# Kernel optimization log

Hardware: AMD Instinct MI355X
Metric: run time of the kernel (lower is better)

## Reference

```python
import jax, jax.numpy as jnp
import numpy as np

N = 50000        # nodes
E = 800000       # edges (before self loops)
F_IN = 64        # num_features
DIM = 64         # num_hidden
C = 10           # num_classes
G = 256          # graphs in batch
NEG_SLOPE = 0.2


def setup_inputs() -> dict:
    key = jax.random.key(0)
    ks = jax.random.split(key, 20)
    def w(k, shape, fan_in):
        return jax.random.normal(k, shape, dtype=jnp.float32) / np.sqrt(fan_in)
    x = jax.random.normal(ks[0], (N, F_IN), dtype=jnp.float32)
    edge_index = jax.random.randint(ks[1], (2, E), 0, N, dtype=jnp.int64)
    batch = jnp.sort(jax.random.randint(ks[2], (N,), 0, G, dtype=jnp.int64))
    return {
        "x": x, "edge_index": edge_index, "batch": batch,
        "w1": w(ks[3], (F_IN, DIM), F_IN), "as1": w(ks[4], (DIM,), DIM), "ad1": w(ks[5], (DIM,), DIM), "b1": jnp.zeros((DIM,), jnp.float32),
        "w2": w(ks[6], (DIM, DIM), DIM),  "as2": w(ks[7], (DIM,), DIM), "ad2": w(ks[8], (DIM,), DIM), "b2": jnp.zeros((DIM,), jnp.float32),
        "w3": w(ks[9], (DIM, DIM), DIM),  "as3": w(ks[10], (DIM,), DIM), "ad3": w(ks[11], (DIM,), DIM), "b3": jnp.zeros((DIM,), jnp.float32),
        "fc1_w": w(ks[12], (DIM, DIM), DIM), "fc1_b": jnp.zeros((DIM,), jnp.float32),
        "fc2_w": w(ks[13], (DIM, C), DIM),   "fc2_b": jnp.zeros((C,), jnp.float32),
    }


def _gat_conv(x, src, dst, w, a_src, a_dst, b, n_nodes):
    # PyG GATConv, heads=1: h = x W; e_ij = LeakyReLU(a_src.h_j + a_dst.h_i);
    # alpha = segment-softmax over edges grouped by target i; out_i = sum_j alpha_ij h_j + b
    h = x @ w                                   # [N, DIM]
    alpha_s = h @ a_src                         # [N]
    alpha_d = h @ a_dst                         # [N]
    e = jax.nn.leaky_relu(alpha_s[src] + alpha_d[dst], NEG_SLOPE)  # [E']
    e_max = jax.ops.segment_max(e, dst, num_segments=n_nodes)
    e_exp = jnp.exp(e - e_max[dst])
    denom = jax.ops.segment_sum(e_exp, dst, num_segments=n_nodes)
    alpha = e_exp / (denom[dst] + 1e-16)        # [E']
    out = jax.ops.segment_sum(alpha[:, None] * h[src], dst, num_segments=n_nodes)
    return out + b


def _l2_normalize(x):
    nrm = jnp.linalg.norm(x, axis=1, keepdims=True)
    return x / jnp.maximum(nrm, 1e-12)


def reference(x, edge_index, batch, w1, as1, ad1, b1, w2, as2, ad2, b2,
              w3, as3, ad3, b3, fc1_w, fc1_b, fc2_w, fc2_b):
    n = x.shape[0]
    loops = jnp.arange(n, dtype=edge_index.dtype)
    src = jnp.concatenate([edge_index[0], loops])   # add_self_loops=True (PyG default)
    dst = jnp.concatenate([edge_index[1], loops])
    h = _gat_conv(x, src, dst, w1, as1, ad1, b1, n)
    h = jax.nn.relu(_l2_normalize(h))
    h = _gat_conv(h, src, dst, w2, as2, ad2, b2, n)
    h = jax.nn.relu(_l2_normalize(h))
    h = _gat_conv(h, src, dst, w3, as3, ad3, b3, n)
    h = jax.nn.relu(_l2_normalize(h))
    g = jax.ops.segment_sum(h, batch, num_segments=G)   # global_add_pool -> [G, DIM]
    g = jax.nn.relu(g @ fc1_w + fc1_b)
    logits = g @ fc2_w + fc2_b
    return jax.nn.log_softmax(logits, axis=-1)
```

## Files before the change

kernel.cpp:

```cpp
#include <hip/hip_runtime.h>
#include <hip/hip_bf16.h>
#include <math.h>

#define DIM 64
#define GNUM 256
#define CNUM 10

__device__ __forceinline__ unsigned bfpack(float a, float b) {
    unsigned ua = __builtin_bit_cast(unsigned, a);
    unsigned ub = __builtin_bit_cast(unsigned, b);
    ua += 0x7fffu + ((ua >> 16) & 1u);
    ub += 0x7fffu + ((ub >> 16) & 1u);
    return (ua >> 16) | (ub & 0xffff0000u);
}
__device__ __forceinline__ float bflo(unsigned u) { return __builtin_bit_cast(float, u << 16); }
__device__ __forceinline__ float bfhi(unsigned u) { return __builtin_bit_cast(float, u & 0xffff0000u); }

__global__ void deg_rank_kernel(const int* __restrict__ ei, int E, int N,
                                int* __restrict__ deg, int* __restrict__ rank) {
    int i = blockIdx.x * blockDim.x + threadIdx.x;
    int EP = E + N;
    if (i >= EP) return;
    int d = (i < E) ? ei[E + i] : (i - E);
    rank[i] = atomicAdd(&deg[d], 1);
}

__global__ __launch_bounds__(256) void scan_misc(const int* __restrict__ deg, int* __restrict__ part, int n, int nb,
                                                 const int* __restrict__ batch, int N,
                                                 int* __restrict__ gstart) {
    int bid = blockIdx.x;
    if (bid < nb) {
        __shared__ int ws[4];
        int i = bid * 256 + threadIdx.x;
        int v = (i < n) ? deg[i] : 0;
        #pragma unroll
        for (int d = 32; d >= 1; d >>= 1) v += __shfl_xor(v, d);
        if ((threadIdx.x & 63) == 0) ws[threadIdx.x >> 6] = v;
        __syncthreads();
        if (threadIdx.x == 0) part[bid] = ws[0] + ws[1] + ws[2] + ws[3];
    } else {
        for (int g = threadIdx.x; g <= GNUM; g += 256) {
            int lo = 0, hi = N;
            while (lo < hi) { int mid = (lo + hi) >> 1; if (batch[mid] < g) lo = mid + 1; else hi = mid; }
            gstart[g] = lo;
        }
    }
}

__global__ __launch_bounds__(256) void scan_down(const int* __restrict__ deg, const int* __restrict__ part,
                                                 int* __restrict__ offs, int n) {
    __shared__ int ws[4];
    __shared__ int base_s;
    int tid = threadIdx.x, lane = tid & 63, wid = tid >> 6;
    int pv = (tid < (int)blockIdx.x) ? part[tid] : 0;
    #pragma unroll
    for (int d = 32; d >= 1; d >>= 1) pv += __shfl_xor(pv, d);
    if (lane == 0) ws[wid] = pv;
    __syncthreads();
    if (tid == 0) base_s = ws[0] + ws[1] + ws[2] + ws[3];
    __syncthreads();
    int i = blockIdx.x * 256 + tid;
    int v = (i < n) ? deg[i] : 0;
    int x = v;
    #pragma unroll
    for (int d = 1; d < 64; d <<= 1) { int t = __shfl_up(x, d); if (lane >= d) x += t; }
    if (lane == 63) ws[wid] = x;
    __syncthreads();
    int add = base_s;
    for (int w = 0; w < wid; ++w) add += ws[w];
    if (i < n) offs[i] = add + x - v;
    if (i == n - 1) offs[n] = add + x;
}

#define XSTR 68
__device__ __forceinline__ void mm_tile_body(int bid,
                                             const float* __restrict__ in, const float* __restrict__ W,
                                             const float* __restrict__ a_s, const float* __restrict__ a_d,
                                             unsigned* __restrict__ hb, float* __restrict__ as_,
                                             float* __restrict__ ad_, int N) {
    __shared__ float Ws[DIM * DIM];
    __shared__ float xT[XSTR * DIM];
    int tid = threadIdx.x;
    int base = bid * 64;

    const float4* W4 = (const float4*)W;
    float4* Ws4 = (float4*)Ws;
    #pragma unroll
    for (int i = 0; i < 4; ++i) Ws4[tid + 256 * i] = W4[tid + 256 * i];

    {
        int row = tid >> 2;
        int kb = (tid & 3) << 4;
        int grow = base + row;
        int crow = grow < N ? grow : N - 1;
        const float4* xr = (const float4*)(in + ((size_t)crow << 6) + kb);
        float4 v0 = xr[0], v1 = xr[1], v2 = xr[2], v3 = xr[3];
        xT[(kb + 0) * XSTR + row] = v0.x;  xT[(kb + 1) * XSTR + row] = v0.y;
        xT[(kb + 2) * XSTR + row] = v0.z;  xT[(kb + 3) * XSTR + row] = v0.w;
        xT[(kb + 4) * XSTR + row] = v1.x;  xT[(kb + 5) * XSTR + row] = v1.y;
        xT[(kb + 6) * XSTR + row] = v1.z;  xT[(kb + 7) * XSTR + row] = v1.w;
        xT[(kb + 8) * XSTR + row] = v2.x;  xT[(kb + 9) * XSTR + row] = v2.y;
        xT[(kb + 10) * XSTR + row] = v2.z; xT[(kb + 11) * XSTR + row] = v2.w;
        xT[(kb + 12) * XSTR + row] = v3.x; xT[(kb + 13) * XSTR + row] = v3.y;
        xT[(kb + 14) * XSTR + row] = v3.z; xT[(kb + 15) * XSTR + row] = v3.w;
    }
    __syncthreads();

    int tx = tid & 15, ty = tid >> 4;
    int c0 = tx << 2, r0 = ty << 2;
    float acc[4][4] = {{0.f}};
    #pragma unroll 8
    for (int k = 0; k < DIM; ++k) {
        float4 xv = *(const float4*)(xT + k * XSTR + r0);
        float4 wv = *(const float4*)(Ws + k * DIM + c0);
        acc[0][0] += xv.x * wv.x; acc[0][1] += xv.x * wv.y; acc[0][2] += xv.x * wv.z; acc[0][3] += xv.x * wv.w;
        acc[1][0] += xv.y * wv.x; acc[1][1] += xv.y * wv.y; acc[1][2] += xv.y * wv.z; acc[1][3] += xv.y * wv.w;
        acc[2][0] += xv.z * wv.x; acc[2][1] += xv.z * wv.y; acc[2][2] += xv.z * wv.z; acc[2][3] += xv.z * wv.w;
        acc[3][0] += xv.w * wv.x; acc[3][1] += xv.w * wv.y; acc[3][2] += xv.w * wv.z; acc[3][3] += xv.w * wv.w;
    }

    float4 av = *(const float4*)(a_s + c0);
    float4 dv = *(const float4*)(a_d + c0);
    #pragma unroll
    for (int ri = 0; ri < 4; ++ri) {
        int grow = base + r0 + ri;
        float s1 = acc[ri][0] * av.x + acc[ri][1] * av.y + acc[ri][2] * av.z + acc[ri][3] * av.w;
        float s2 = acc[ri][0] * dv.x + acc[ri][1] * dv.y + acc[ri][2] * dv.z + acc[ri][3] * dv.w;
        #pragma unroll
        for (int d = 1; d <= 8; d <<= 1) { s1 += __shfl_xor(s1, d); s2 += __shfl_xor(s2, d); }
        if (grow < N) {
            uint2 o;
            o.x = bfpack(acc[ri][0], acc[ri][1]);
            o.y = bfpack(acc[ri][2], acc[ri][3]);
            *(uint2*)(hb + ((size_t)grow << 5) + (tx << 1)) = o;
            if (tx == 0) { as_[grow] = s1; ad_[grow] = s2; }
        }
    }
}

__global__ __launch_bounds__(256) void mm_tile(const float* __restrict__ in, const float* __restrict__ W,
                                               const float* __restrict__ a_s, const float* __restrict__ a_d,
                                               unsigned* __restrict__ hb, float* __restrict__ as_,
                                               float* __restrict__ ad_, int N) {
    mm_tile_body(blockIdx.x, in, W, a_s, a_d, hb, as_, ad_, N);
}

__global__ __launch_bounds__(256) void mm_fill(const float* __restrict__ in, const float* __restrict__ W,
                                               const float* __restrict__ a_s, const float* __restrict__ a_d,
                                               unsigned* __restrict__ hb, float* __restrict__ as_,
                                               float* __restrict__ ad_, int N, int nbt,
                                               const int* __restrict__ ei, const int* __restrict__ rank, int E,
                                               const int* __restrict__ offs, int* __restrict__ csr_src) {
    int bid = blockIdx.x;
    if (bid < nbt) {
        mm_tile_body(bid, in, W, a_s, a_d, hb, as_, ad_, N);
    } else {
        int i = (bid - nbt) * 256 + threadIdx.x;
        int EP = E + N;
        if (i >= EP) return;
        int s, d;
        if (i < E) { s = ei[i]; d = ei[E + i]; } else { s = i - E; d = i - E; }
        csr_src[offs[d] + rank[i]] = s;
    }
}

__global__ __launch_bounds__(256) void gat_agg(const unsigned* __restrict__ hb, const float* __restrict__ as_,
                                               const float* __restrict__ ad_, const int* __restrict__ offs,
                                               const int* __restrict__ csr, const float* __restrict__ bias,
                                               float* __restrict__ out, int N) {
    int tid = threadIdx.x, lane = tid & 63, wid = tid >> 6;
    int node = blockIdx.x * 4 + wid;
    if (node >= N) return;
    int start = offs[node], end = offs[node + 1];
    int deg = end - start;
    float adi = ad_[node];

    int src_reg = 0;
    float e_reg = -1e30f;
    if (lane < deg) {
        src_reg = csr[start + lane];
        float e = as_[src_reg] + adi;
        e_reg = (e > 0.f) ? e : 0.2f * e;
    }
    float m = e_reg;
    for (int t = start + 64 + lane; t < end; t += 64) {
        float e = as_[csr[t]] + adi;
        e = (e > 0.f) ? e : 0.2f * e;
        m = fmaxf(m, e);
    }
    #pragma unroll
    for (int d = 32; d >= 1; d >>= 1) m = fmaxf(m, __shfl_xor(m, d));

    float w_reg = (lane < deg) ? expf(e_reg - m) : 0.f;
    float s = w_reg;
    for (int t = start + 64 + lane; t < end; t += 64) {
        float e = as_[csr[t]] + adi;
        e = (e > 0.f) ? e : 0.2f * e;
        s += expf(e - m);
    }
    #pragma unroll
    for (int d = 32; d >= 1; d >>= 1) s += __shfl_xor(s, d);

    int esub = lane >> 4, fg = lane & 15;
    int dmain = deg < 64 ? deg : 64;
    float a0 = 0.f, a1 = 0.f, a2 = 0.f, a3 = 0.f;
    for (int i0 = 0; i0 < dmain; i0 += 16) {
        float wA = __shfl(w_reg, i0 + esub);
        int   sA = __shfl(src_reg, i0 + esub);
        float wB = __shfl(w_reg, i0 + 4 + esub);
        int   sB = __shfl(src_reg, i0 + 4 + esub);
        float wC = __shfl(w_reg, i0 + 8 + esub);
        int   sC = __shfl(src_reg, i0 + 8 + esub);
        float wD = __shfl(w_reg, i0 + 12 + esub);
        int   sD = __shfl(src_reg, i0 + 12 + esub);
        const uint2 hA = *(const uint2*)(hb + ((size_t)sA << 5) + (fg << 1));
        const uint2 hB = *(const uint2*)(hb + ((size_t)sB << 5) + (fg << 1));
        const uint2 hC = *(const uint2*)(hb + ((size_t)sC << 5) + (fg << 1));
        const uint2 hD = *(const uint2*)(hb + ((size_t)sD << 5) + (fg << 1));
        a0 += wA * bflo(hA.x) + wB * bflo(hB.x) + wC * bflo(hC.x) + wD * bflo(hD.x);
        a1 += wA * bfhi(hA.x) + wB * bfhi(hB.x) + wC * bfhi(hC.x) + wD * bfhi(hD.x);
        a2 += wA * bflo(hA.y) + wB * bflo(hB.y) + wC * bflo(hC.y) + wD * bflo(hD.y);
        a3 += wA * bfhi(hA.y) + wB * bfhi(hB.y) + wC * bfhi(hC.y) + wD * bfhi(hD.y);
    }
    for (int t0 = start + 64; t0 < end; t0 += 4) {
        int t = t0 + esub;
        float w = 0.f; int src = 0;
        if (t < end) {
            src = csr[t];
            float e = as_[src] + adi;
            e = (e > 0.f) ? e : 0.2f * e;
            w = expf(e - m);
        }
        const uint2 hv = *(const uint2*)(hb + ((size_t)src << 5) + (fg << 1));
        a0 += w * bflo(hv.x); a1 += w * bfhi(hv.x);
        a2 += w * bflo(hv.y); a3 += w * bfhi(hv.y);
    }
    #pragma unroll
    for (int d = 16; d <= 32; d <<= 1) {
        a0 += __shfl_xor(a0, d); a1 += __shfl_xor(a1, d);
        a2 += __shfl_xor(a2, d); a3 += __shfl_xor(a3, d);
    }
    float inv = 1.f / (s + 1e-16f);
    const float4 bv = *(const float4*)(bias + (fg << 2));
    float o0 = a0 * inv + bv.x, o1 = a1 * inv + bv.y, o2 = a2 * inv + bv.z, o3 = a3 * inv + bv.w;
    float n2 = o0 * o0 + o1 * o1 + o2 * o2 + o3 * o3;
    #pragma unroll
    for (int d = 1; d <= 8; d <<= 1) n2 += __shfl_xor(n2, d);
    float innrm = 1.f / fmaxf(sqrtf(n2), 1e-12f);
    if (esub == 0) {
        float4 o;
        o.x = fmaxf(o0 * innrm, 0.f); o.y = fmaxf(o1 * innrm, 0.f);
        o.z = fmaxf(o2 * innrm, 0.f); o.w = fmaxf(o3 * innrm, 0.f);
        *(float4*)(out + ((size_t)node << 6) + (fg << 2)) = o;
    }
}

__global__ __launch_bounds__(256) void pool_mlp(const float* __restrict__ h, const int* __restrict__ gstart,
                                                const float* __restrict__ fc1w, const float* __restrict__ fc1b,
                                                const float* __restrict__ fc2w, const float* __restrict__ fc2b,
                                                float* __restrict__ out) {
    __shared__ float W1[DIM * DIM];
    __shared__ float red[4 * DIM];
    __shared__ float tbuf[DIM];
    __shared__ float obuf[CNUM];
    int tid = threadIdx.x, lane = tid & 63, wv = tid >> 6;
    int gid = blockIdx.x;

    const float4* W4 = (const float4*)fc1w;
    float4* W1s = (float4*)W1;
    #pragma unroll
    for (int i = 0; i < 4; ++i) W1s[tid + 256 * i] = W4[tid + 256 * i];

    int s = gstart[gid], e = gstart[gid + 1];
    float acc = 0.f;
    for (int i = s + wv; i < e; i += 4) acc += h[((size_t)i << 6) + lane];
    red[wv * DIM + lane] = acc;
    __syncthreads();

    if (wv == 0) {
        float g = red[lane] + red[DIM + lane] + red[2 * DIM + lane] + red[3 * DIM + lane];
        float t = fc1b[lane];
        #pragma unroll
        for (int k = 0; k < DIM; ++k) t += __shfl(g, k) * W1[k * DIM + lane];
        t = fmaxf(t, 0.f);
        tbuf[lane] = t;
        float o = 0.f;
        if (lane < CNUM) {
            o = fc2b[lane];
            #pragma unroll
            for (int k = 0; k < DIM; ++k) o += tbuf[k] * fc2w[k * CNUM + lane];
            obuf[lane] = o;
        }
        if (lane < CNUM) {
            float mx = obuf[0];
            #pragma unroll
            for (int k = 1; k < CNUM; ++k) mx = fmaxf(mx, obuf[k]);
            float ssum = 0.f;
            #pragma unroll
            for (int k = 0; k < CNUM; ++k) ssum += expf(obuf[k] - mx);
            out[gid * CNUM + lane] = o - mx - logf(ssum);
        }
    }
}

static inline size_t align256(size_t x) { return (x + 255) & ~size_t(255); }

extern "C" void kernel_launch(void* const* d_in, const int* in_sizes, int n_in,
                              void* d_out, int out_size, void* d_ws, size_t ws_size,
                              hipStream_t stream) {
    const float* x     = (const float*)d_in[0];
    const int*   ei    = (const int*)d_in[1];
    const int*   batch = (const int*)d_in[2];
    const float* w1  = (const float*)d_in[3];
    const float* as1 = (const float*)d_in[4];
    const float* ad1 = (const float*)d_in[5];
    const float* b1  = (const float*)d_in[6];
    const float* w2  = (const float*)d_in[7];
    const float* as2 = (const float*)d_in[8];
    const float* ad2 = (const float*)d_in[9];
    const float* b2  = (const float*)d_in[10];
    const float* w3  = (const float*)d_in[11];
    const float* as3 = (const float*)d_in[12];
    const float* ad3 = (const float*)d_in[13];
    const float* b3  = (const float*)d_in[14];
    const float* fc1w = (const float*)d_in[15];
    const float* fc1b = (const float*)d_in[16];
    const float* fc2w = (const float*)d_in[17];
    const float* fc2b = (const float*)d_in[18];
    float* out = (float*)d_out;

    int N  = in_sizes[0] / DIM;
    int E  = in_sizes[1] / 2;
    int EP = E + N;
    int nb = (N + 255) / 256;

    char* p = (char*)d_ws;
    unsigned* hbf = (unsigned*)p; p += align256(sizeof(unsigned) * (size_t)N * (DIM / 2));
    float* oA   = (float*)p; p += align256(sizeof(float) * (size_t)N * DIM);
    float* oB   = (float*)p; p += align256(sizeof(float) * (size_t)N * DIM);
    float* as_  = (float*)p; p += align256(sizeof(float) * (size_t)N);
    float* ad_  = (float*)p; p += align256(sizeof(float) * (size_t)N);
    int*   deg  = (int*)p;   p += align256(sizeof(int) * (size_t)N);
    int*   offs = (int*)p;   p += align256(sizeof(int) * (size_t)(N + 1));
    int*   rank = (int*)p;   p += align256(sizeof(int) * (size_t)EP);
    int*   csr  = (int*)p;   p += align256(sizeof(int) * (size_t)EP);
    int*   part = (int*)p;   p += align256(sizeof(int) * (size_t)nb);
    int*   gst  = (int*)p;   p += align256(sizeof(int) * (size_t)(GNUM + 1));

    int nblk = (N + 3) / 4;
    int nbt = (N + 63) / 64;
    int epBlocks = (EP + 255) / 256;

    hipMemsetAsync(deg, 0, sizeof(int) * (size_t)N, stream);
    deg_rank_kernel<<<epBlocks, 256, 0, stream>>>(ei, E, N, deg, rank);
    scan_misc<<<nb + 1, 256, 0, stream>>>(deg, part, N, nb, batch, N, gst);
    scan_down<<<nb, 256, 0, stream>>>(deg, part, offs, N);

    mm_fill<<<nbt + epBlocks, 256, 0, stream>>>(x, w1, as1, ad1, hbf, as_, ad_, N, nbt,
                                                ei, rank, E, offs, csr);
    gat_agg<<<nblk, 256, 0, stream>>>(hbf, as_, ad_, offs, csr, b1, oA, N);
    mm_tile<<<nbt, 256, 0, stream>>>(oA, w2, as2, ad2, hbf, as_, ad_, N);
    gat_agg<<<nblk, 256, 0, stream>>>(hbf, as_, ad_, offs, csr, b2, oB, N);
    mm_tile<<<nbt, 256, 0, stream>>>(oB, w3, as3, ad3, hbf, as_, ad_, N);
    gat_agg<<<nblk, 256, 0, stream>>>(hbf, as_, ad_, offs, csr, b3, oA, N);

    pool_mlp<<<GNUM, 256, 0, stream>>>(oA, gst, fc1w, fc1b, fc2w, fc2b, out);
}
```

Before: 290.2 us.

## Store inter-layer activations as bf16 and drop softmax max pass

The GAT aggregation now writes its normalized, ReLU'd output as packed bf16 instead of fp32. The following matmul tiles and the pooling kernel read bf16 directly, which halves the intermediate activation traffic. The segment softmax no longer computes a per-node max or a separate denominator pass. It exponentiates raw logits and accumulates the sum inside the gather loop, removing the shuffle reductions and the extra loops over high-degree nodes. The cost is lower precision in intermediates and a possible exp overflow if attention logits get large.

```diff
diff --git a/kernel.cpp b/kernel.cpp
--- a/kernel.cpp
+++ b/kernel.cpp
@@ -15,6 +15,7 @@
 }
 __device__ __forceinline__ float bflo(unsigned u) { return __builtin_bit_cast(float, u << 16); }
 __device__ __forceinline__ float bfhi(unsigned u) { return __builtin_bit_cast(float, u & 0xffff0000u); }
+__device__ __forceinline__ float bfs(unsigned short u) { return __builtin_bit_cast(float, (unsigned)u << 16); }
 
 __global__ void deg_rank_kernel(const int* __restrict__ ei, int E, int N,
                                 int* __restrict__ deg, int* __restrict__ rank) {
@@ -73,8 +74,9 @@
 }
 
 #define XSTR 68
+template<bool BF16IN>
 __device__ __forceinline__ void mm_tile_body(int bid,
-                                             const float* __restrict__ in, const float* __restrict__ W,
+                                             const void* __restrict__ in_, const float* __restrict__ W,
                                              const float* __restrict__ a_s, const float* __restrict__ a_d,
                                              unsigned* __restrict__ hb, float* __restrict__ as_,
                                              float* __restrict__ ad_, int N) {
@@ -93,16 +95,30 @@
         int kb = (tid & 3) << 4;
         int grow = base + row;
         int crow = grow < N ? grow : N - 1;
-        const float4* xr = (const float4*)(in + ((size_t)crow << 6) + kb);
-        float4 v0 = xr[0], v1 = xr[1], v2 = xr[2], v3 = xr[3];
-        xT[(kb + 0) * XSTR + row] = v0.x;  xT[(kb + 1) * XSTR + row] = v0.y;
-        xT[(kb + 2) * XSTR + row] = v0.z;  xT[(kb + 3) * XSTR + row] = v0.w;
-        xT[(kb + 4) * XSTR + row] = v1.x;  xT[(kb + 5) * XSTR + row] = v1.y;
-        xT[(kb + 6) * XSTR + row] = v1.z;  xT[(kb + 7) * XSTR + row] = v1.w;
-        xT[(kb + 8) * XSTR + row] = v2.x;  xT[(kb + 9) * XSTR + row] = v2.y;
-        xT[(kb + 10) * XSTR + row] = v2.z; xT[(kb + 11) * XSTR + row] = v2.w;
-        xT[(kb + 12) * XSTR + row] = v3.x; xT[(kb + 13) * XSTR + row] = v3.y;
-        xT[(kb + 14) * XSTR + row] = v3.z; xT[(kb + 15) * XSTR + row] = v3.w;
+        if (BF16IN) {
+            const unsigned* xr = (const unsigned*)in_ + ((size_t)crow << 5) + (kb >> 1);
+            uint4 u0 = *(const uint4*)xr;
+            uint4 u1 = *(const uint4*)(xr + 4);
+            xT[(kb + 0) * XSTR + row] = bflo(u0.x);  xT[(kb + 1) * XSTR + row] = bfhi(u0.x);
+            xT[(kb + 2) * XSTR + row] = bflo(u0.y);  xT[(kb + 3) * XSTR + row] = bfhi(u0.y);
+            xT[(kb + 4) * XSTR + row] = bflo(u0.z);  xT[(kb + 5) * XSTR + row] = bfhi(u0.z);
+            xT[(kb + 6) * XSTR + row] = bflo(u0.w);  xT[(kb + 7) * XSTR + row] = bfhi(u0.w);
+            xT[(kb + 8) * XSTR + row] = bflo(u1.x);  xT[(kb + 9) * XSTR + row] = bfhi(u1.x);
+            xT[(kb + 10) * XSTR + row] = bflo(u1.y); xT[(kb + 11) * XSTR + row] = bfhi(u1.y);
+            xT[(kb + 12) * XSTR + row] = bflo(u1.z); xT[(kb + 13) * XSTR + row] = bfhi(u1.z);
+            xT[(kb + 14) * XSTR + row] = bflo(u1.w); xT[(kb + 15) * XSTR + row] = bfhi(u1.w);
+        } else {
+            const float4* xr = (const float4*)((const float*)in_ + ((size_t)crow << 6) + kb);
+            float4 v0 = xr[0], v1 = xr[1], v2 = xr[2], v3 = xr[3];
+            xT[(kb + 0) * XSTR + row] = v0.x;  xT[(kb + 1) * XSTR + row] = v0.y;
+            xT[(kb + 2) * XSTR + row] = v0.z;  xT[(kb + 3) * XSTR + row] = v0.w;
+            xT[(kb + 4) * XSTR + row] = v1.x;  xT[(kb + 5) * XSTR + row] = v1.y;
+            xT[(kb + 6) * XSTR + row] = v1.z;  xT[(kb + 7) * XSTR + row] = v1.w;
+            xT[(kb + 8) * XSTR + row] = v2.x;  xT[(kb + 9) * XSTR + row] = v2.y;
+            xT[(kb + 10) * XSTR + row] = v2.z; xT[(kb + 11) * XSTR + row] = v2.w;
+            xT[(kb + 12) * XSTR + row] = v3.x; xT[(kb + 13) * XSTR + row] = v3.y;
+            xT[(kb + 14) * XSTR + row] = v3.z; xT[(kb + 15) * XSTR + row] = v3.w;
+        }
     }
     __syncthreads();
 
@@ -138,11 +154,11 @@
     }
 }
 
-__global__ __launch_bounds__(256) void mm_tile(const float* __restrict__ in, const float* __restrict__ W,
-                                               const float* __restrict__ a_s, const float* __restrict__ a_d,
-                                               unsigned* __restrict__ hb, float* __restrict__ as_,
-                                               float* __restrict__ ad_, int N) {
-    mm_tile_body(blockIdx.x, in, W, a_s, a_d, hb, as_, ad_, N);
+__global__ __launch_bounds__(256) void mm_tile_bf(const unsigned* __restrict__ in, const float* __restrict__ W,
+                                                  const float* __restrict__ a_s, const float* __restrict__ a_d,
+                                                  unsigned* __restrict__ hb, float* __restrict__ as_,
+                                                  float* __restrict__ ad_, int N) {
+    mm_tile_body<true>(blockIdx.x, in, W, a_s, a_d, hb, as_, ad_, N);
 }
 
 __global__ __launch_bounds__(256) void mm_fill(const float* __restrict__ in, const float* __restrict__ W,
@@ -153,7 +169,7 @@
                                                const int* __restrict__ offs, int* __restrict__ csr_src) {
     int bid = blockIdx.x;
     if (bid < nbt) {
-        mm_tile_body(bid, in, W, a_s, a_d, hb, as_, ad_, N);
+        mm_tile_body<false>(bid, in, W, a_s, a_d, hb, as_, ad_, N);
     } else {
         int i = (bid - nbt) * 256 + threadIdx.x;
         int EP = E + N;
@@ -167,7 +183,7 @@
 __global__ __launch_bounds__(256) void gat_agg(const unsigned* __restrict__ hb, const float* __restrict__ as_,
                                                const float* __restrict__ ad_, const int* __restrict__ offs,
                                                const int* __restrict__ csr, const float* __restrict__ bias,
-                                               float* __restrict__ out, int N) {
+                                               unsigned* __restrict__ outb, int N) {
     int tid = threadIdx.x, lane = tid & 63, wid = tid >> 6;
     int node = blockIdx.x * 4 + wid;
     if (node >= N) return;
@@ -176,34 +192,17 @@
     float adi = ad_[node];
 
     int src_reg = 0;
-    float e_reg = -1e30f;
+    float w_reg = 0.f;
     if (lane < deg) {
         src_reg = csr[start + lane];
         float e = as_[src_reg] + adi;
-        e_reg = (e > 0.f) ? e : 0.2f * e;
-    }
-    float m = e_reg;
-    for (int t = start + 64 + lane; t < end; t += 64) {
-        float e = as_[csr[t]] + adi;
         e = (e > 0.f) ? e : 0.2f * e;
-        m = fmaxf(m, e);
-    }
-    #pragma unroll
-    for (int d = 32; d >= 1; d >>= 1) m = fmaxf(m, __shfl_xor(m, d));
-
-    float w_reg = (lane < deg) ? expf(e_reg - m) : 0.f;
-    float s = w_reg;
-    for (int t = start + 64 + lane; t < end; t += 64) {
-        float e = as_[csr[t]] + adi;
-        e = (e > 0.f) ? e : 0.2f * e;
-        s += expf(e - m);
-    }
-    #pragma unroll
-    for (int d = 32; d >= 1; d >>= 1) s += __shfl_xor(s, d);
+        w_reg = expf(e);
+    }
 
     int esub = lane >> 4, fg = lane & 15;
     int dmain = deg < 64 ? deg : 64;
-    float a0 = 0.f, a1 = 0.f, a2 = 0.f, a3 = 0.f;
+    float a0 = 0.f, a1 = 0.f, a2 = 0.f, a3 = 0.f, sw = 0.f;
     for (int i0 = 0; i0 < dmain; i0 += 16) {
         float wA = __shfl(w_reg, i0 + esub);
         int   sA = __shfl(src_reg, i0 + esub);
@@ -217,6 +216,7 @@
         const uint2 hB = *(const uint2*)(hb + ((size_t)sB << 5) + (fg << 1));
         const uint2 hC = *(const uint2*)(hb + ((size_t)sC << 5) + (fg << 1));
         const uint2 hD = *(const uint2*)(hb + ((size_t)sD << 5) + (fg << 1));
+        sw += wA + wB + wC + wD;
         a0 += wA * bflo(hA.x) + wB * bflo(hB.x) + wC * bflo(hC.x) + wD * bflo(hD.x);
         a1 += wA * bfhi(hA.x) + wB * bfhi(hB.x) + wC * bfhi(hC.x) + wD * bfhi(hD.x);
         a2 += wA * bflo(hA.y) + wB * bflo(hB.y) + wC * bflo(hC.y) + wD * bflo(hD.y);
@@ -229,9 +229,10 @@
             src = csr[t];
             float e = as_[src] + adi;
             e = (e > 0.f) ? e : 0.2f * e;
-            w = expf(e - m);
+            w = expf(e);
         }
         const uint2 hv = *(const uint2*)(hb + ((size_t)src << 5) + (fg << 1));
+        sw += w;
         a0 += w * bflo(hv.x); a1 += w * bfhi(hv.x);
         a2 += w * bflo(hv.y); a3 += w * bfhi(hv.y);
     }
@@ -239,8 +240,9 @@
     for (int d = 16; d <= 32; d <<= 1) {
         a0 += __shfl_xor(a0, d); a1 += __shfl_xor(a1, d);
         a2 += __shfl_xor(a2, d); a3 += __shfl_xor(a3, d);
-    }
-    float inv = 1.f / (s + 1e-16f);
+        sw += __shfl_xor(sw, d);
+    }
+    float inv = 1.f / (sw + 1e-16f);
     const float4 bv = *(const float4*)(bias + (fg << 2));
     float o0 = a0 * inv + bv.x, o1 = a1 * inv + bv.y, o2 = a2 * inv + bv.z, o3 = a3 * inv + bv.w;
     float n2 = o0 * o0 + o1 * o1 + o2 * o2 + o3 * o3;
@@ -248,14 +250,14 @@
     for (int d = 1; d <= 8; d <<= 1) n2 += __shfl_xor(n2, d);
     float innrm = 1.f / fmaxf(sqrtf(n2), 1e-12f);
     if (esub == 0) {
-        float4 o;
-        o.x = fmaxf(o0 * innrm, 0.f); o.y = fmaxf(o1 * innrm, 0.f);
-        o.z = fmaxf(o2 * innrm, 0.f); o.w = fmaxf(o3 * innrm, 0.f);
-        *(float4*)(out + ((size_t)node << 6) + (fg << 2)) = o;
-    }
-}
-
-__global__ __launch_bounds__(256) void pool_mlp(const float* __restrict__ h, const int* __restrict__ gstart,
+        uint2 o;
+        o.x = bfpack(fmaxf(o0 * innrm, 0.f), fmaxf(o1 * innrm, 0.f));
+        o.y = bfpack(fmaxf(o2 * innrm, 0.f), fmaxf(o3 * innrm, 0.f));
+        *(uint2*)(outb + ((size_t)node << 5) + (fg << 1)) = o;
+    }
+}
+
+__global__ __launch_bounds__(256) void pool_mlp(const unsigned short* __restrict__ hb, const int* __restrict__ gstart,
                                                 const float* __restrict__ fc1w, const float* __restrict__ fc1b,
                                                 const float* __restrict__ fc2w, const float* __restrict__ fc2b,
                                                 float* __restrict__ out) {
@@ -273,7 +275,7 @@
 
     int s = gstart[gid], e = gstart[gid + 1];
     float acc = 0.f;
-    for (int i = s + wv; i < e; i += 4) acc += h[((size_t)i << 6) + lane];
+    for (int i = s + wv; i < e; i += 4) acc += bfs(hb[((size_t)i << 6) + lane]);
     red[wv * DIM + lane] = acc;
     __syncthreads();
 
@@ -336,8 +338,8 @@
 
     char* p = (char*)d_ws;
     unsigned* hbf = (unsigned*)p; p += align256(sizeof(unsigned) * (size_t)N * (DIM / 2));
-    float* oA   = (float*)p; p += align256(sizeof(float) * (size_t)N * DIM);
-    float* oB   = (float*)p; p += align256(sizeof(float) * (size_t)N * DIM);
+    unsigned* oAb = (unsigned*)p; p += align256(sizeof(unsigned) * (size_t)N * (DIM / 2));
+    unsigned* oBb = (unsigned*)p; p += align256(sizeof(unsigned) * (size_t)N * (DIM / 2));
     float* as_  = (float*)p; p += align256(sizeof(float) * (size_t)N);
     float* ad_  = (float*)p; p += align256(sizeof(float) * (size_t)N);
     int*   deg  = (int*)p;   p += align256(sizeof(int) * (size_t)N);
@@ -358,11 +360,11 @@
 
     mm_fill<<<nbt + epBlocks, 256, 0, stream>>>(x, w1, as1, ad1, hbf, as_, ad_, N, nbt,
                                                 ei, rank, E, offs, csr);
-    gat_agg<<<nblk, 256, 0, stream>>>(hbf, as_, ad_, offs, csr, b1, oA, N);
-    mm_tile<<<nbt, 256, 0, stream>>>(oA, w2, as2, ad2, hbf, as_, ad_, N);
-    gat_agg<<<nblk, 256, 0, stream>>>(hbf, as_, ad_, offs, csr, b2, oB, N);
-    mm_tile<<<nbt, 256, 0, stream>>>(oB, w3, as3, ad3, hbf, as_, ad_, N);
-    gat_agg<<<nblk, 256, 0, stream>>>(hbf, as_, ad_, offs, csr, b3, oA, N);
-
-    pool_mlp<<<GNUM, 256, 0, stream>>>(oA, gst, fc1w, fc1b, fc2w, fc2b, out);
-}
+    gat_agg<<<nblk, 256, 0, stream>>>(hbf, as_, ad_, offs, csr, b1, oAb, N);
+    mm_tile_bf<<<nbt, 256, 0, stream>>>(oAb, w2, as2, ad2, hbf, as_, ad_, N);
+    gat_agg<<<nblk, 256, 0, stream>>>(hbf, as_, ad_, offs, csr, b2, oBb, N);
+    mm_tile_bf<<<nbt, 256, 0, stream>>>(oBb, w3, as3, ad3, hbf, as_, ad_, N);
+    gat_agg<<<nblk, 256, 0, stream>>>(hbf, as_, ad_, offs, csr, b3, oAb, N);
+
+    pool_mlp<<<GNUM, 256, 0, stream>>>((const unsigned short*)oAb, gst, fc1w, fc1b, fc2w, fc2b, out);
+}
```

New measurement: 283.9 us, median of 2. 1.02x faster.
